# Kernel tuning notes

Measured on AMD Instinct MI355X. Metric: run time of the kernel, lower is better.

Reference implementation:

```python
import jax, jax.numpy as jnp
import numpy as np

N = 100_000  # nodes
E = 1_200_000  # edges (avg degree 12)
EPS = 1e-5


def setup_inputs() -> dict:
    key = jax.random.key(0)
    ks = jax.random.split(key, 12)

    def w(k, shape):
        fan_in = shape[0]
        return jax.random.normal(k, shape, dtype=jnp.float32) * (1.0 / np.sqrt(fan_in))

    return {
        "x": jax.random.normal(ks[0], (N, 4), dtype=jnp.float32),
        "edge_index": jax.random.randint(ks[1], (2, E), 0, N, dtype=jnp.int32),
        "W1": w(ks[2], (4, 16)), "b1": jnp.zeros(16, jnp.float32),
        "g1": jnp.ones(16, jnp.float32), "bt1": jnp.zeros(16, jnp.float32),
        "W2": w(ks[3], (16, 32)), "b2": jnp.zeros(32, jnp.float32),
        "g2": jnp.ones(32, jnp.float32), "bt2": jnp.zeros(32, jnp.float32),
        "W3": w(ks[4], (32, 64)), "b3": jnp.zeros(64, jnp.float32),
        "g3": jnp.ones(64, jnp.float32), "bt3": jnp.zeros(64, jnp.float32),
        "Wf1": w(ks[5], (64, 32)), "bf1": jnp.zeros(32, jnp.float32),
        "Wf2": w(ks[6], (32, 16)), "bf2": jnp.zeros(16, jnp.float32),
        "Wf3": w(ks[7], (16, 2)), "bf3": jnp.zeros(2, jnp.float32),
    }


def _gcn_conv(x, W, b, src, dst):
    """PyG GCNConv: self-loops + symmetric deg^-1/2 normalization + scatter-add."""
    n = x.shape[0]
    h = x @ W  # [N, out]
    loop = jnp.arange(n, dtype=src.dtype)
    s = jnp.concatenate([src, loop])  # [E+N]
    d = jnp.concatenate([dst, loop])
    deg = jax.ops.segment_sum(jnp.ones_like(d, dtype=h.dtype), d, num_segments=n)
    dinv = jnp.where(deg > 0, jax.lax.rsqrt(deg), 0.0)
    norm = dinv[s] * dinv[d]  # [E+N]
    out = jax.ops.segment_sum(h[s] * norm[:, None], d, num_segments=n)
    return out + b


def _bn(x, g, bt):
    # BatchNorm1d over node dim (batch statistics, training-mode semantics)
    m = jnp.mean(x, axis=0)
    v = jnp.var(x, axis=0)
    return (x - m) * jax.lax.rsqrt(v + EPS) * g + bt


def reference(x, edge_index, W1, b1, g1, bt1, W2, b2, g2, bt2, W3, b3, g3, bt3,
              Wf1, bf1, Wf2, bf2, Wf3, bf3):
    src, dst = edge_index[0], edge_index[1]
    h = jax.nn.elu(_bn(jax.nn.relu(_gcn_conv(x, W1, b1, src, dst)), g1, bt1))
    h = jax.nn.elu(_bn(jax.nn.relu(_gcn_conv(h, W2, b2, src, dst)), g2, bt2))
    h = jax.nn.elu(_bn(jax.nn.relu(_gcn_conv(h, W3, b3, src, dst)), g3, bt3))
    h = jax.nn.elu(h @ Wf1 + bf1)
    h = jax.nn.elu(h @ Wf2 + bf2)
    h = h @ Wf3 + bf3
    return jax.nn.log_softmax(h, axis=1)
```

## Files before the change

### kernel.cpp

```cpp
#include <hip/hip_runtime.h>
#include <hip/hip_fp16.h>
#include <math.h>

#define BN_EPS 1e-5f

union H8 {
  float4 f4;
  __half2 h2[4];
};


#define NHB 512

__global__ void hist_kernel(const int* __restrict__ dst, int* __restrict__ histpart, int e) {
  __shared__ int h[512];
  for (int i = threadIdx.x; i < 512; i += 256) h[i] = 0;
  __syncthreads();
  int stride = gridDim.x * 256;
  for (int i = blockIdx.x * 256 + threadIdx.x; i < e; i += stride)
    atomicAdd(&h[dst[i] >> 8], 1);
  __syncthreads();
  for (int i = threadIdx.x; i < 512; i += 256)
    histpart[blockIdx.x * 512 + i] = h[i];
}

__global__ void scan_buckets(const int* __restrict__ histpart,
                             int* __restrict__ boffset, int* __restrict__ bcursor,
                             int* __restrict__ row_start, int nbuck, int n, int e) {
  __shared__ int sc[512];
  int tid = threadIdx.x;
  int v = 0;
  for (int r = 0; r < NHB; r++) v += histpart[r * 512 + tid];
  sc[tid] = v;
  __syncthreads();
  for (int off = 1; off < 512; off <<= 1) {
    int add = (tid >= off) ? sc[tid - off] : 0;
    __syncthreads();
    sc[tid] += add;
    __syncthreads();
  }
  int excl = sc[tid] - v;
  if (tid <= nbuck) {
    int val = (tid < nbuck) ? excl : e;
    boffset[tid] = val;
    bcursor[tid] = val;
  }
  if (tid == 0) row_start[n] = e;
}

__global__ void partition_kernel(const int* __restrict__ src, const int* __restrict__ dst,
                                 int* __restrict__ bcursor, int* __restrict__ ebuf, int e) {
  __shared__ int h[512];
  __shared__ int base[512];
  const int BLK_E = 4096;
  int e0 = blockIdx.x * BLK_E;
  int e1 = min(e0 + BLK_E, e);
  for (int i = threadIdx.x; i < 512; i += 256) h[i] = 0;
  __syncthreads();
  for (int i = e0 + threadIdx.x; i < e1; i += 256)
    atomicAdd(&h[dst[i] >> 8], 1);
  __syncthreads();
  for (int i = threadIdx.x; i < 512; i += 256) {
    int c = h[i];
    base[i] = (c > 0) ? atomicAdd(&bcursor[i], c) : 0;
    h[i] = 0;
  }
  __syncthreads();
  for (int i = e0 + threadIdx.x; i < e1; i += 256) {
    int d = dst[i];
    int b = d >> 8;
    int r = atomicAdd(&h[b], 1);
    ebuf[base[b] + r] = (src[i] << 8) | (d & 255);
  }
}

__global__ void bucket_fill(const int* __restrict__ ebuf, const int* __restrict__ boffset,
                            int* __restrict__ row_start, float* __restrict__ dinv,
                            int* __restrict__ csr_src, int n) {
  __shared__ int lcnt[256];
  __shared__ int lpre[256];
  int bid = blockIdx.x;
  int nb0 = bid << 8;
  int tid = threadIdx.x;
  int e0 = boffset[bid], e1 = boffset[bid + 1];
  lcnt[tid] = 0;
  __syncthreads();
  for (int j = e0 + tid; j < e1; j += 256)
    atomicAdd(&lcnt[ebuf[j] & 255], 1);
  __syncthreads();
  int v = lcnt[tid];
  lpre[tid] = v;
  __syncthreads();
  for (int off = 1; off < 256; off <<= 1) {
    int add = (tid >= off) ? lpre[tid - off] : 0;
    __syncthreads();
    lpre[tid] += add;
    __syncthreads();
  }
  int excl = lpre[tid] - v;
  int node = nb0 + tid;
  if (node < n) {
    row_start[node] = e0 + excl;
    dinv[node] = rsqrtf((float)(v + 1));
  }
  __syncthreads();
  lpre[tid] = excl;
  __syncthreads();
  for (int j = e0 + tid; j < e1; j += 256) {
    int ed = ebuf[j];
    int p = atomicAdd(&lpre[ed & 255], 1);
    csr_src[e0 + p] = ed >> 8;
  }
}

template <int K, int C, bool BN>
__global__ __launch_bounds__(256) void mm_dinv_h(
    const float* __restrict__ X, const float* __restrict__ stats,
    const float* __restrict__ g, const float* __restrict__ bt,
    const float* __restrict__ W, const float* __restrict__ dinv,
    float4* __restrict__ hh, int n) {
  constexpr int GP8 = C / 8;
  __shared__ float w[K * C];
  __shared__ float bsc[K], bsh[K];
  for (int i = threadIdx.x; i < K * C; i += 256) w[i] = W[i];
  if (BN && threadIdx.x < K) {
    int c = threadIdx.x;
    float inv_n = 1.0f / (float)n;
    float m = stats[c] * inv_n;
    float var = fmaxf(stats[K + c] * inv_n - m * m, 0.f);
    float sc = rsqrtf(var + BN_EPS) * g[c];
    bsc[c] = sc;
    bsh[c] = bt[c] - m * sc;
  }
  __syncthreads();

  int idx = blockIdx.x * 256 + threadIdx.x;
  if (idx >= n * GP8) return;
  int nn = idx / GP8;
  int c8 = idx % GP8;

  float acc[8];
#pragma unroll
  for (int t = 0; t < 8; t++) acc[t] = 0.f;

  const float4* row4 = (const float4*)(X + (size_t)nn * K);
#pragma unroll
  for (int k4 = 0; k4 < K / 4; k4++) {
    float4 xv = row4[k4];
#pragma unroll
    for (int j = 0; j < 4; j++) {
      int k = k4 * 4 + j;
      float v = (j == 0) ? xv.x : (j == 1) ? xv.y : (j == 2) ? xv.z : xv.w;
      if (BN) {
        v = v * bsc[k] + bsh[k];
        v = v > 0.f ? v : (__expf(v) - 1.f);
      }
      int wb = k * C + c8 * 8;
#pragma unroll
      for (int t = 0; t < 8; t++) acc[t] += v * w[wb + t];
    }
  }
  float dn = dinv[nn];
  H8 o;
#pragma unroll
  for (int q = 0; q < 4; q++)
    o.h2[q] = __float22half2_rn(make_float2(acc[2 * q] * dn, acc[2 * q + 1] * dn));
  hh[idx] = o.f4;
}

template <int C, int LOGGP, bool OUTH>
__global__ __launch_bounds__(256) void gather_finalize_h(
    const float4* __restrict__ hh8, const int* __restrict__ row_start,
    const int* __restrict__ csr_src, const float* __restrict__ dinv,
    const float* __restrict__ bias, float4* __restrict__ act4,
    float* __restrict__ partials, int n) {
  constexpr int GP = C / 8;
  constexpr int GP4 = C / 4;
  constexpr int NPB = 256 / GP;
  int tid = threadIdx.x;
  int c8 = tid & (GP - 1);
  int local = tid >> LOGGP;
  int n0 = blockIdx.x * NPB + local;
  bool valid = (n0 < n);

  float vo[8];
#pragma unroll
  for (int t = 0; t < 8; t++) vo[t] = 0.f;

  if (valid) {
    float acc[8];
    {
      H8 u;
      u.f4 = hh8[n0 * GP + c8];
#pragma unroll
      for (int q = 0; q < 4; q++) {
        float2 f = __half22float2(u.h2[q]);
        acc[2 * q] = f.x;
        acc[2 * q + 1] = f.y;
      }
    }
    int s = row_start[n0], e0 = row_start[n0 + 1];
    int j = s;
    for (; j + 8 <= e0; j += 8) {
      H8 u[8];
#pragma unroll
      for (int m = 0; m < 8; m++) u[m].f4 = hh8[csr_src[j + m] * GP + c8];
#pragma unroll
      for (int m = 0; m < 8; m++)
#pragma unroll
        for (int q = 0; q < 4; q++) {
          float2 f = __half22float2(u[m].h2[q]);
          acc[2 * q] += f.x;
          acc[2 * q + 1] += f.y;
        }
    }
    for (; j + 4 <= e0; j += 4) {
      H8 u[4];
#pragma unroll
      for (int m = 0; m < 4; m++) u[m].f4 = hh8[csr_src[j + m] * GP + c8];
#pragma unroll
      for (int m = 0; m < 4; m++)
#pragma unroll
        for (int q = 0; q < 4; q++) {
          float2 f = __half22float2(u[m].h2[q]);
          acc[2 * q] += f.x;
          acc[2 * q + 1] += f.y;
        }
    }
    for (; j < e0; j++) {
      H8 u;
      u.f4 = hh8[csr_src[j] * GP + c8];
#pragma unroll
      for (int q = 0; q < 4; q++) {
        float2 f = __half22float2(u.h2[q]);
        acc[2 * q] += f.x;
        acc[2 * q + 1] += f.y;
      }
    }

    float dn = dinv[n0];
    const float4* bias4 = (const float4*)bias;
    float4 blo = bias4[c8 * 2], bhi = bias4[c8 * 2 + 1];
    vo[0] = fmaxf(dn * acc[0] + blo.x, 0.f);
    vo[1] = fmaxf(dn * acc[1] + blo.y, 0.f);
    vo[2] = fmaxf(dn * acc[2] + blo.z, 0.f);
    vo[3] = fmaxf(dn * acc[3] + blo.w, 0.f);
    vo[4] = fmaxf(dn * acc[4] + bhi.x, 0.f);
    vo[5] = fmaxf(dn * acc[5] + bhi.y, 0.f);
    vo[6] = fmaxf(dn * acc[6] + bhi.z, 0.f);
    vo[7] = fmaxf(dn * acc[7] + bhi.w, 0.f);
    if (OUTH) {
      H8 o;
#pragma unroll
      for (int q = 0; q < 4; q++)
        o.h2[q] = __float22half2_rn(make_float2(vo[2 * q], vo[2 * q + 1]));
      act4[(size_t)n0 * GP + c8] = o.f4;
    } else {
      act4[n0 * GP4 + c8 * 2] = make_float4(vo[0], vo[1], vo[2], vo[3]);
      act4[n0 * GP4 + c8 * 2 + 1] = make_float4(vo[4], vo[5], vo[6], vo[7]);
    }
  }

  __shared__ float redS[8 * 256];
  __shared__ float redQ[8 * 256];
#pragma unroll
  for (int t = 0; t < 8; t++) {
    redS[t * 256 + tid] = vo[t];
    redQ[t * 256 + tid] = vo[t] * vo[t];
  }
#pragma unroll
  for (int off = NPB / 2; off >= 1; off >>= 1) {
    __syncthreads();
    if (local < off) {
#pragma unroll
      for (int t = 0; t < 8; t++) {
        redS[t * 256 + tid] += redS[t * 256 + tid + off * GP];
        redQ[t * 256 + tid] += redQ[t * 256 + tid + off * GP];
      }
    }
  }
  __syncthreads();
  if (local == 0) {
#pragma unroll
    for (int t = 0; t < 8; t++) {
      partials[(size_t)blockIdx.x * 2 * C + c8 * 8 + t] = redS[t * 256 + tid];
      partials[(size_t)blockIdx.x * 2 * C + C + c8 * 8 + t] = redQ[t * 256 + tid];
    }
  }
}

template <int C2>
__global__ void reduce_partials(const float* __restrict__ partials,
                                float* __restrict__ stats, int rows) {
  int ch = blockIdx.x;
  float acc = 0.f;
  for (int r = threadIdx.x; r < rows; r += 256)
    acc += partials[(size_t)r * C2 + ch];
  __shared__ float red[256];
  red[threadIdx.x] = acc;
  __syncthreads();
#pragma unroll
  for (int off = 128; off >= 1; off >>= 1) {
    if (threadIdx.x < off) red[threadIdx.x] += red[threadIdx.x + off];
    __syncthreads();
  }
  if (threadIdx.x == 0) stats[ch] = red[0];
}


__global__ __launch_bounds__(256) void head_kernel(
    const float4* __restrict__ h16,
    const float* __restrict__ st3, const float* __restrict__ g3,
    const float* __restrict__ bt3,
    const float* __restrict__ Wf1, const float* __restrict__ bf1,
    const float* __restrict__ Wf2, const float* __restrict__ bf2,
    const float* __restrict__ Wf3, const float* __restrict__ bf3,
    float* __restrict__ out, int n) {
  __shared__ float w1[64 * 32], w2[32 * 16], w3[32];
  __shared__ float sb1[32], sb2[16], sb3[2];
  __shared__ float bsc[64], bsh[64];
  __shared__ float a1s[32][128];
  __shared__ float a2s[16][128];
  int tid = threadIdx.x;
  for (int i = tid; i < 64 * 32; i += 256) w1[i] = Wf1[i];
  for (int i = tid; i < 32 * 16; i += 256) w2[i] = Wf2[i];
  if (tid < 64) {
    float inv_n = 1.0f / (float)n;
    float m = st3[tid] * inv_n;
    float var = fmaxf(st3[64 + tid] * inv_n - m * m, 0.f);
    float sc = rsqrtf(var + BN_EPS) * g3[tid];
    bsc[tid] = sc;
    bsh[tid] = bt3[tid] - m * sc;
  }
  if (tid < 32) {
    w3[tid] = Wf3[tid];
    sb1[tid] = bf1[tid];
  }
  if (tid < 16) sb2[tid] = bf2[tid];
  if (tid < 2) sb3[tid] = bf3[tid];
  __syncthreads();

  int node = tid & 127;
  int half = tid >> 7;
  int n0 = blockIdx.x * 128 + node;
  bool valid = (n0 < n);

  float a1[16];
#pragma unroll
  for (int c = 0; c < 16; c++) a1[c] = sb1[half * 16 + c];
  if (valid) {
    const float4* hrow = h16 + (size_t)n0 * 8;
#pragma unroll
    for (int j = 0; j < 8; j++) {
      H8 u;
      u.f4 = hrow[j];
#pragma unroll
      for (int q = 0; q < 4; q++) {
        float2 f = __half22float2(u.h2[q]);
        int k0 = j * 8 + 2 * q, k1 = k0 + 1;
        float v0 = f.x * bsc[k0] + bsh[k0];
        v0 = v0 > 0.f ? v0 : (__expf(v0) - 1.f);
        float v1 = f.y * bsc[k1] + bsh[k1];
        v1 = v1 > 0.f ? v1 : (__expf(v1) - 1.f);
#pragma unroll
        for (int c = 0; c < 16; c++)
          a1[c] += v0 * w1[k0 * 32 + half * 16 + c] + v1 * w1[k1 * 32 + half * 16 + c];
      }
    }
  }
#pragma unroll
  for (int c = 0; c < 16; c++) {
    float v = a1[c];
    a1s[half * 16 + c][node] = v > 0.f ? v : (__expf(v) - 1.f);
  }
  __syncthreads();

  float a2[8];
#pragma unroll
  for (int c = 0; c < 8; c++) a2[c] = sb2[half * 8 + c];
#pragma unroll
  for (int k = 0; k < 32; k++) {
    float ak = a1s[k][node];
#pragma unroll
    for (int c = 0; c < 8; c++) a2[c] += ak * w2[k * 16 + half * 8 + c];
  }
#pragma unroll
  for (int c = 0; c < 8; c++) {
    float v = a2[c];
    a2s[half * 8 + c][node] = v > 0.f ? v : (__expf(v) - 1.f);
  }
  __syncthreads();

  if (half == 0 && valid) {
    float z0 = sb3[0], z1 = sb3[1];
#pragma unroll
    for (int k = 0; k < 16; k++) {
      float ak = a2s[k][node];
      z0 += ak * w3[k * 2 + 0];
      z1 += ak * w3[k * 2 + 1];
    }
    float mx = fmaxf(z0, z1);
    float lse = mx + __logf(__expf(z0 - mx) + __expf(z1 - mx));
    out[(size_t)n0 * 2 + 0] = z0 - lse;
    out[(size_t)n0 * 2 + 1] = z1 - lse;
  }
}


extern "C" void kernel_launch(void* const* d_in, const int* in_sizes, int n_in,
                              void* d_out, int out_size, void* d_ws, size_t ws_size,
                              hipStream_t stream) {
  const float* x = (const float*)d_in[0];
  const int* ei = (const int*)d_in[1];
  const float* W1 = (const float*)d_in[2];  const float* b1 = (const float*)d_in[3];
  const float* g1 = (const float*)d_in[4];  const float* bt1 = (const float*)d_in[5];
  const float* W2 = (const float*)d_in[6];  const float* b2 = (const float*)d_in[7];
  const float* g2 = (const float*)d_in[8];  const float* bt2 = (const float*)d_in[9];
  const float* W3 = (const float*)d_in[10]; const float* b3 = (const float*)d_in[11];
  const float* g3 = (const float*)d_in[12]; const float* bt3 = (const float*)d_in[13];
  const float* Wf1 = (const float*)d_in[14]; const float* bf1 = (const float*)d_in[15];
  const float* Wf2 = (const float*)d_in[16]; const float* bf2 = (const float*)d_in[17];
  const float* Wf3 = (const float*)d_in[18]; const float* bf3 = (const float*)d_in[19];
  float* out = (float*)d_out;

  const int N = in_sizes[0] / 4;
  const int E = in_sizes[1] / 2;
  const int* srcp = ei;
  const int* dstp = ei + E;
  const int NBUCK = (N + 255) >> 8;

  char* ws = (char*)d_ws;
  size_t off = 0;
  auto alloc = [&](size_t bytes) {
    off = (off + 255) & ~(size_t)255;
    size_t o = off;
    off += bytes;
    return o;
  };
  float* dinv      = (float*)(ws + alloc((size_t)N * 4));
  int*   row_start = (int*)  (ws + alloc((size_t)(N + 1) * 4));
  int*   histpart  = (int*)  (ws + alloc((size_t)NHB * 512 * 4));
  float* stats     = (float*)(ws + alloc((size_t)224 * 4));
  int*   boffset   = (int*)  (ws + alloc((size_t)513 * 4));
  int*   bcursor   = (int*)  (ws + alloc((size_t)513 * 4));
  int*   csr_src   = (int*)  (ws + alloc((size_t)E * 4));
  float* partials  = (float*)(ws + alloc((size_t)3200 * 128 * 4));
  float* bufH      = (float*)(ws + alloc((size_t)N * 64 * 2));
  float* bufAct    = (float*)(ws + alloc((size_t)N * 64 * 4));
  float* st1 = stats;
  float* st2 = stats + 32;
  float* st3 = stats + 96;
  int*   ebuf = (int*)bufH;

  hist_kernel<<<NHB, 256, 0, stream>>>(dstp, histpart, E);
  scan_buckets<<<1, 512, 0, stream>>>(histpart, boffset, bcursor, row_start, NBUCK, N, E);
  partition_kernel<<<(E + 4095) / 4096, 256, 0, stream>>>(srcp, dstp, bcursor, ebuf, E);
  bucket_fill<<<NBUCK, 256, 0, stream>>>(ebuf, boffset, row_start, dinv, csr_src, N);

  int g1n = (N + 127) / 128;
  mm_dinv_h<4, 16, false><<<(N * 2 + 255) / 256, 256, 0, stream>>>(
      x, nullptr, nullptr, nullptr, W1, dinv, (float4*)bufH, N);
  gather_finalize_h<16, 1, false><<<g1n, 256, 0, stream>>>(
      (const float4*)bufH, row_start, csr_src, dinv, b1, (float4*)bufAct, partials, N);
  reduce_partials<32><<<32, 256, 0, stream>>>(partials, st1, g1n);

  int g2n = (N + 63) / 64;
  mm_dinv_h<16, 32, true><<<(N * 4 + 255) / 256, 256, 0, stream>>>(
      bufAct, st1, g1, bt1, W2, dinv, (float4*)bufH, N);
  gather_finalize_h<32, 2, false><<<g2n, 256, 0, stream>>>(
      (const float4*)bufH, row_start, csr_src, dinv, b2, (float4*)bufAct, partials, N);
  reduce_partials<64><<<64, 256, 0, stream>>>(partials, st2, g2n);

  int g3n = (N + 31) / 32;
  mm_dinv_h<32, 64, true><<<(N * 8 + 255) / 256, 256, 0, stream>>>(
      bufAct, st2, g2, bt2, W3, dinv, (float4*)bufH, N);
  gather_finalize_h<64, 3, true><<<g3n, 256, 0, stream>>>(
      (const float4*)bufH, row_start, csr_src, dinv, b3, (float4*)bufAct, partials, N);
  reduce_partials<128><<<128, 256, 0, stream>>>(partials, st3, g3n);

  head_kernel<<<(N + 127) / 128, 256, 0, stream>>>(
      (const float4*)bufAct, st3, g3, bt3, Wf1, bf1, Wf2, bf2, Wf3, bf3, out, N);
}
```

Baseline: 198.4 us.

## Aggregate before matmul in GCN layers to gather narrower features

Uses linearity of the GCN aggregation to gather the input features (width K) before multiplying by W, rather than gathering the transformed features (width C). This halves the bytes moved per edge in each layer's gather. The layer-1 input scaling is folded into bucket_fill, and a separate prep_y kernel applies BN+ELU+dinv. BN statistics now come from a separate stats_h pass using atomics instead of per-block partials plus a reduce kernel. Activations are stored in fp16 throughout, which adds an extra read pass per layer for stats and prep.

```diff
diff --git a/kernel.cpp b/kernel.cpp
--- a/kernel.cpp
+++ b/kernel.cpp
@@ -8,6 +8,10 @@
   float4 f4;
   __half2 h2[4];
 };
+union H4 {
+  uint2 u2;
+  __half2 h2[2];
+};
 
 
 #define NHB 512
@@ -26,9 +30,11 @@
 
 __global__ void scan_buckets(const int* __restrict__ histpart,
                              int* __restrict__ boffset, int* __restrict__ bcursor,
-                             int* __restrict__ row_start, int nbuck, int n, int e) {
+                             int* __restrict__ row_start, float* __restrict__ stats,
+                             int nbuck, int n, int e) {
   __shared__ int sc[512];
   int tid = threadIdx.x;
+  if (tid < 224) stats[tid] = 0.f;
   int v = 0;
   for (int r = 0; r < NHB; r++) v += histpart[r * 512 + tid];
   sc[tid] = v;
@@ -75,8 +81,9 @@
 }
 
 __global__ void bucket_fill(const int* __restrict__ ebuf, const int* __restrict__ boffset,
+                            const float* __restrict__ x,
                             int* __restrict__ row_start, float* __restrict__ dinv,
-                            int* __restrict__ csr_src, int n) {
+                            int* __restrict__ csr_src, uint2* __restrict__ y1, int n) {
   __shared__ int lcnt[256];
   __shared__ int lpre[256];
   int bid = blockIdx.x;
@@ -101,7 +108,13 @@
   int node = nb0 + tid;
   if (node < n) {
     row_start[node] = e0 + excl;
-    dinv[node] = rsqrtf((float)(v + 1));
+    float dnv = rsqrtf((float)(v + 1));
+    dinv[node] = dnv;
+    float4 xr = ((const float4*)x)[node];
+    H4 o;
+    o.h2[0] = __float22half2_rn(make_float2(xr.x * dnv, xr.y * dnv));
+    o.h2[1] = __float22half2_rn(make_float2(xr.z * dnv, xr.w * dnv));
+    y1[node] = o.u2;
   }
   __syncthreads();
   lpre[tid] = excl;
@@ -113,198 +126,222 @@
   }
 }
 
-template <int K, int C, bool BN>
-__global__ __launch_bounds__(256) void mm_dinv_h(
-    const float* __restrict__ X, const float* __restrict__ stats,
-    const float* __restrict__ g, const float* __restrict__ bt,
-    const float* __restrict__ W, const float* __restrict__ dinv,
-    float4* __restrict__ hh, int n) {
-  constexpr int GP8 = C / 8;
-  __shared__ float w[K * C];
-  __shared__ float bsc[K], bsh[K];
-  for (int i = threadIdx.x; i < K * C; i += 256) w[i] = W[i];
-  if (BN && threadIdx.x < K) {
+template <int K, int C, int LOGG>
+__global__ __launch_bounds__(256) void gather_mm(
+    const void* __restrict__ yv, const int* __restrict__ row_start,
+    const int* __restrict__ csr_src, const float* __restrict__ dinv,
+    const float* __restrict__ Wg, const float* __restrict__ bias,
+    float4* __restrict__ act4, int n) {
+  constexpr int G = 1 << LOGG;
+  constexpr int NPB = 256 >> LOGG;
+  constexpr int KG = (K >= 8) ? K / 8 : 1;
+  __shared__ __align__(16) float w[K * C];
+  __shared__ float sb[C];
+  __shared__ float s_lds[K][NPB + 1];
+  int tid = threadIdx.x;
+  for (int i = tid; i < K * C; i += 256) w[i] = Wg[i];
+  if (tid < C) sb[tid] = bias[tid];
+  int g = tid & (G - 1);
+  int local = tid >> LOGG;
+  int n0 = blockIdx.x * NPB + local;
+  bool valid = (n0 < n);
+
+  if (K == 4) {
+    const uint2* y4 = (const uint2*)yv;
+    float s0 = 0.f, s1 = 0.f, s2 = 0.f, s3 = 0.f;
+    if (valid) {
+      H4 u;
+      u.u2 = y4[n0];
+      float2 a = __half22float2(u.h2[0]), b = __half22float2(u.h2[1]);
+      s0 = a.x; s1 = a.y; s2 = b.x; s3 = b.y;
+      int st = row_start[n0], e0 = row_start[n0 + 1];
+      int j = st;
+      for (; j + 8 <= e0; j += 8) {
+        H4 u8[8];
+#pragma unroll
+        for (int m = 0; m < 8; m++) u8[m].u2 = y4[csr_src[j + m]];
+#pragma unroll
+        for (int m = 0; m < 8; m++) {
+          float2 p = __half22float2(u8[m].h2[0]), q = __half22float2(u8[m].h2[1]);
+          s0 += p.x; s1 += p.y; s2 += q.x; s3 += q.y;
+        }
+      }
+      for (; j < e0; j++) {
+        H4 u1;
+        u1.u2 = y4[csr_src[j]];
+        float2 p = __half22float2(u1.h2[0]), q = __half22float2(u1.h2[1]);
+        s0 += p.x; s1 += p.y; s2 += q.x; s3 += q.y;
+      }
+    }
+    s_lds[0][local] = s0; s_lds[1][local] = s1;
+    s_lds[2][local] = s2; s_lds[3][local] = s3;
+  } else {
+    const float4* y8 = (const float4*)yv;
+    float s[8];
+#pragma unroll
+    for (int t = 0; t < 8; t++) s[t] = 0.f;
+    if (valid) {
+      H8 u;
+      u.f4 = y8[(size_t)n0 * KG + g];
+#pragma unroll
+      for (int q = 0; q < 4; q++) {
+        float2 f = __half22float2(u.h2[q]);
+        s[2 * q] = f.x; s[2 * q + 1] = f.y;
+      }
+      int st = row_start[n0], e0 = row_start[n0 + 1];
+      int j = st;
+      for (; j + 8 <= e0; j += 8) {
+        H8 u8[8];
+#pragma unroll
+        for (int m = 0; m < 8; m++) u8[m].f4 = y8[(size_t)csr_src[j + m] * KG + g];
+#pragma unroll
+        for (int m = 0; m < 8; m++)
+#pragma unroll
+          for (int q = 0; q < 4; q++) {
+            float2 f = __half22float2(u8[m].h2[q]);
+            s[2 * q] += f.x; s[2 * q + 1] += f.y;
+          }
+      }
+      for (; j + 4 <= e0; j += 4) {
+        H8 u4[4];
+#pragma unroll
+        for (int m = 0; m < 4; m++) u4[m].f4 = y8[(size_t)csr_src[j + m] * KG + g];
+#pragma unroll
+        for (int m = 0; m < 4; m++)
+#pragma unroll
+          for (int q = 0; q < 4; q++) {
+            float2 f = __half22float2(u4[m].h2[q]);
+            s[2 * q] += f.x; s[2 * q + 1] += f.y;
+          }
+      }
+      for (; j < e0; j++) {
+        H8 u1;
+        u1.f4 = y8[(size_t)csr_src[j] * KG + g];
+#pragma unroll
+        for (int q = 0; q < 4; q++) {
+          float2 f = __half22float2(u1.h2[q]);
+          s[2 * q] += f.x; s[2 * q + 1] += f.y;
+        }
+      }
+    }
+#pragma unroll
+    for (int t = 0; t < 8; t++) s_lds[g * 8 + t][local] = s[t];
+  }
+  __syncthreads();
+
+  if (!valid) return;
+  float dn = dinv[n0];
+  float acc[16];
+#pragma unroll
+  for (int c = 0; c < 16; c++) acc[c] = 0.f;
+#pragma unroll
+  for (int k = 0; k < K; k++) {
+    float ak = s_lds[k][local];
+    const float4* wr = (const float4*)&w[k * C + g * 16];
+    float4 w0 = wr[0], w1 = wr[1], w2 = wr[2], w3 = wr[3];
+    acc[0] += ak * w0.x;  acc[1] += ak * w0.y;  acc[2] += ak * w0.z;  acc[3] += ak * w0.w;
+    acc[4] += ak * w1.x;  acc[5] += ak * w1.y;  acc[6] += ak * w1.z;  acc[7] += ak * w1.w;
+    acc[8] += ak * w2.x;  acc[9] += ak * w2.y;  acc[10] += ak * w2.z; acc[11] += ak * w2.w;
+    acc[12] += ak * w3.x; acc[13] += ak * w3.y; acc[14] += ak * w3.z; acc[15] += ak * w3.w;
+  }
+  H8 o0, o1;
+#pragma unroll
+  for (int q = 0; q < 4; q++) {
+    float v0 = fmaxf(dn * acc[2 * q] + sb[g * 16 + 2 * q], 0.f);
+    float v1 = fmaxf(dn * acc[2 * q + 1] + sb[g * 16 + 2 * q + 1], 0.f);
+    o0.h2[q] = __float22half2_rn(make_float2(v0, v1));
+    float v2 = fmaxf(dn * acc[8 + 2 * q] + sb[g * 16 + 8 + 2 * q], 0.f);
+    float v3 = fmaxf(dn * acc[8 + 2 * q + 1] + sb[g * 16 + 8 + 2 * q + 1], 0.f);
+    o1.h2[q] = __float22half2_rn(make_float2(v2, v3));
+  }
+  act4[(size_t)n0 * (C / 8) + g * 2] = o0.f4;
+  act4[(size_t)n0 * (C / 8) + g * 2 + 1] = o1.f4;
+}
+
+template <int C>
+__global__ __launch_bounds__(256) void stats_h(const float4* __restrict__ act4,
+                                               float* __restrict__ stats, int n) {
+  constexpr int GP = C / 8;
+  constexpr int NPB = 256 / GP;
+  int tid = threadIdx.x;
+  int c8 = tid & (GP - 1);
+  int local = tid / GP;
+  float s[8], q[8];
+#pragma unroll
+  for (int t = 0; t < 8; t++) { s[t] = 0.f; q[t] = 0.f; }
+  for (int n0 = blockIdx.x * NPB + local; n0 < n; n0 += gridDim.x * NPB) {
+    H8 u;
+    u.f4 = act4[(size_t)n0 * GP + c8];
+#pragma unroll
+    for (int p = 0; p < 4; p++) {
+      float2 f = __half22float2(u.h2[p]);
+      s[2 * p] += f.x;      s[2 * p + 1] += f.y;
+      q[2 * p] += f.x * f.x; q[2 * p + 1] += f.y * f.y;
+    }
+  }
+  __shared__ float redS[8 * 256];
+  __shared__ float redQ[8 * 256];
+#pragma unroll
+  for (int t = 0; t < 8; t++) {
+    redS[t * 256 + tid] = s[t];
+    redQ[t * 256 + tid] = q[t];
+  }
+#pragma unroll
+  for (int off = NPB / 2; off >= 1; off >>= 1) {
+    __syncthreads();
+    if (local < off) {
+#pragma unroll
+      for (int t = 0; t < 8; t++) {
+        redS[t * 256 + tid] += redS[t * 256 + tid + off * GP];
+        redQ[t * 256 + tid] += redQ[t * 256 + tid + off * GP];
+      }
+    }
+  }
+  __syncthreads();
+  if (local == 0) {
+#pragma unroll
+    for (int t = 0; t < 8; t++) {
+      atomicAdd(&stats[c8 * 8 + t], redS[t * 256 + tid]);
+      atomicAdd(&stats[C + c8 * 8 + t], redQ[t * 256 + tid]);
+    }
+  }
+}
+
+template <int C>
+__global__ __launch_bounds__(256) void prep_y(
+    const float4* __restrict__ act4, const float* __restrict__ stats,
+    const float* __restrict__ gg, const float* __restrict__ bt,
+    const float* __restrict__ dinv, float4* __restrict__ y, int n) {
+  constexpr int GP = C / 8;
+  __shared__ float bsc[C], bsh[C];
+  if (threadIdx.x < C) {
     int c = threadIdx.x;
     float inv_n = 1.0f / (float)n;
     float m = stats[c] * inv_n;
-    float var = fmaxf(stats[K + c] * inv_n - m * m, 0.f);
-    float sc = rsqrtf(var + BN_EPS) * g[c];
+    float var = fmaxf(stats[C + c] * inv_n - m * m, 0.f);
+    float sc = rsqrtf(var + BN_EPS) * gg[c];
     bsc[c] = sc;
     bsh[c] = bt[c] - m * sc;
   }
   __syncthreads();
-
   int idx = blockIdx.x * 256 + threadIdx.x;
-  if (idx >= n * GP8) return;
-  int nn = idx / GP8;
-  int c8 = idx % GP8;
-
-  float acc[8];
-#pragma unroll
-  for (int t = 0; t < 8; t++) acc[t] = 0.f;
-
-  const float4* row4 = (const float4*)(X + (size_t)nn * K);
-#pragma unroll
-  for (int k4 = 0; k4 < K / 4; k4++) {
-    float4 xv = row4[k4];
-#pragma unroll
-    for (int j = 0; j < 4; j++) {
-      int k = k4 * 4 + j;
-      float v = (j == 0) ? xv.x : (j == 1) ? xv.y : (j == 2) ? xv.z : xv.w;
-      if (BN) {
-        v = v * bsc[k] + bsh[k];
-        v = v > 0.f ? v : (__expf(v) - 1.f);
-      }
-      int wb = k * C + c8 * 8;
-#pragma unroll
-      for (int t = 0; t < 8; t++) acc[t] += v * w[wb + t];
-    }
-  }
+  if (idx >= n * GP) return;
+  int nn = idx / GP;
+  int c8 = idx % GP;
   float dn = dinv[nn];
-  H8 o;
-#pragma unroll
-  for (int q = 0; q < 4; q++)
-    o.h2[q] = __float22half2_rn(make_float2(acc[2 * q] * dn, acc[2 * q + 1] * dn));
-  hh[idx] = o.f4;
-}
-
-template <int C, int LOGGP, bool OUTH>
-__global__ __launch_bounds__(256) void gather_finalize_h(
-    const float4* __restrict__ hh8, const int* __restrict__ row_start,
-    const int* __restrict__ csr_src, const float* __restrict__ dinv,
-    const float* __restrict__ bias, float4* __restrict__ act4,
-    float* __restrict__ partials, int n) {
-  constexpr int GP = C / 8;
-  constexpr int GP4 = C / 4;
-  constexpr int NPB = 256 / GP;
-  int tid = threadIdx.x;
-  int c8 = tid & (GP - 1);
-  int local = tid >> LOGGP;
-  int n0 = blockIdx.x * NPB + local;
-  bool valid = (n0 < n);
-
-  float vo[8];
-#pragma unroll
-  for (int t = 0; t < 8; t++) vo[t] = 0.f;
-
-  if (valid) {
-    float acc[8];
-    {
-      H8 u;
-      u.f4 = hh8[n0 * GP + c8];
-#pragma unroll
-      for (int q = 0; q < 4; q++) {
-        float2 f = __half22float2(u.h2[q]);
-        acc[2 * q] = f.x;
-        acc[2 * q + 1] = f.y;
-      }
-    }
-    int s = row_start[n0], e0 = row_start[n0 + 1];
-    int j = s;
-    for (; j + 8 <= e0; j += 8) {
-      H8 u[8];
-#pragma unroll
-      for (int m = 0; m < 8; m++) u[m].f4 = hh8[csr_src[j + m] * GP + c8];
-#pragma unroll
-      for (int m = 0; m < 8; m++)
-#pragma unroll
-        for (int q = 0; q < 4; q++) {
-          float2 f = __half22float2(u[m].h2[q]);
-          acc[2 * q] += f.x;
-          acc[2 * q + 1] += f.y;
-        }
-    }
-    for (; j + 4 <= e0; j += 4) {
-      H8 u[4];
-#pragma unroll
-      for (int m = 0; m < 4; m++) u[m].f4 = hh8[csr_src[j + m] * GP + c8];
-#pragma unroll
-      for (int m = 0; m < 4; m++)
-#pragma unroll
-        for (int q = 0; q < 4; q++) {
-          float2 f = __half22float2(u[m].h2[q]);
-          acc[2 * q] += f.x;
-          acc[2 * q + 1] += f.y;
-        }
-    }
-    for (; j < e0; j++) {
-      H8 u;
-      u.f4 = hh8[csr_src[j] * GP + c8];
-#pragma unroll
-      for (int q = 0; q < 4; q++) {
-        float2 f = __half22float2(u.h2[q]);
-        acc[2 * q] += f.x;
-        acc[2 * q + 1] += f.y;
-      }
-    }
-
-    float dn = dinv[n0];
-    const float4* bias4 = (const float4*)bias;
-    float4 blo = bias4[c8 * 2], bhi = bias4[c8 * 2 + 1];
-    vo[0] = fmaxf(dn * acc[0] + blo.x, 0.f);
-    vo[1] = fmaxf(dn * acc[1] + blo.y, 0.f);
-    vo[2] = fmaxf(dn * acc[2] + blo.z, 0.f);
-    vo[3] = fmaxf(dn * acc[3] + blo.w, 0.f);
-    vo[4] = fmaxf(dn * acc[4] + bhi.x, 0.f);
-    vo[5] = fmaxf(dn * acc[5] + bhi.y, 0.f);
-    vo[6] = fmaxf(dn * acc[6] + bhi.z, 0.f);
-    vo[7] = fmaxf(dn * acc[7] + bhi.w, 0.f);
-    if (OUTH) {
-      H8 o;
-#pragma unroll
-      for (int q = 0; q < 4; q++)
-        o.h2[q] = __float22half2_rn(make_float2(vo[2 * q], vo[2 * q + 1]));
-      act4[(size_t)n0 * GP + c8] = o.f4;
-    } else {
-      act4[n0 * GP4 + c8 * 2] = make_float4(vo[0], vo[1], vo[2], vo[3]);
-      act4[n0 * GP4 + c8 * 2 + 1] = make_float4(vo[4], vo[5], vo[6], vo[7]);
-    }
-  }
-
-  __shared__ float redS[8 * 256];
-  __shared__ float redQ[8 * 256];
-#pragma unroll
-  for (int t = 0; t < 8; t++) {
-    redS[t * 256 + tid] = vo[t];
-    redQ[t * 256 + tid] = vo[t] * vo[t];
-  }
-#pragma unroll
-  for (int off = NPB / 2; off >= 1; off >>= 1) {
-    __syncthreads();
-    if (local < off) {
-#pragma unroll
-      for (int t = 0; t < 8; t++) {
-        redS[t * 256 + tid] += redS[t * 256 + tid + off * GP];
-        redQ[t * 256 + tid] += redQ[t * 256 + tid + off * GP];
-      }
-    }
-  }
-  __syncthreads();
-  if (local == 0) {
-#pragma unroll
-    for (int t = 0; t < 8; t++) {
-      partials[(size_t)blockIdx.x * 2 * C + c8 * 8 + t] = redS[t * 256 + tid];
-      partials[(size_t)blockIdx.x * 2 * C + C + c8 * 8 + t] = redQ[t * 256 + tid];
-    }
-  }
-}
-
-template <int C2>
-__global__ void reduce_partials(const float* __restrict__ partials,
-                                float* __restrict__ stats, int rows) {
-  int ch = blockIdx.x;
-  float acc = 0.f;
-  for (int r = threadIdx.x; r < rows; r += 256)
-    acc += partials[(size_t)r * C2 + ch];
-  __shared__ float red[256];
-  red[threadIdx.x] = acc;
-  __syncthreads();
-#pragma unroll
-  for (int off = 128; off >= 1; off >>= 1) {
-    if (threadIdx.x < off) red[threadIdx.x] += red[threadIdx.x + off];
-    __syncthreads();
-  }
-  if (threadIdx.x == 0) stats[ch] = red[0];
+  H8 u, o;
+  u.f4 = act4[idx];
+#pragma unroll
+  for (int p = 0; p < 4; p++) {
+    float2 f = __half22float2(u.h2[p]);
+    int k0 = c8 * 8 + 2 * p, k1 = k0 + 1;
+    float v0 = f.x * bsc[k0] + bsh[k0];
+    v0 = v0 > 0.f ? v0 : (__expf(v0) - 1.f);
+    float v1 = f.y * bsc[k1] + bsh[k1];
+    v1 = v1 > 0.f ? v1 : (__expf(v1) - 1.f);
+    o.h2[p] = __float22half2_rn(make_float2(v0 * dn, v1 * dn));
+  }
+  y[idx] = o.f4;
 }
 
 
@@ -444,40 +481,36 @@
   int*   boffset   = (int*)  (ws + alloc((size_t)513 * 4));
   int*   bcursor   = (int*)  (ws + alloc((size_t)513 * 4));
   int*   csr_src   = (int*)  (ws + alloc((size_t)E * 4));
-  float* partials  = (float*)(ws + alloc((size_t)3200 * 128 * 4));
-  float* bufH      = (float*)(ws + alloc((size_t)N * 64 * 2));
-  float* bufAct    = (float*)(ws + alloc((size_t)N * 64 * 4));
+  uint2* y1        = (uint2*)(ws + alloc((size_t)N * 8));
+  float* ybuf      = (float*)(ws + alloc((size_t)N * 32 * 2));
+  float* act       = (float*)(ws + alloc((size_t)N * 64 * 2));
   float* st1 = stats;
   float* st2 = stats + 32;
   float* st3 = stats + 96;
-  int*   ebuf = (int*)bufH;
+  int*   ebuf = (int*)act;
 
   hist_kernel<<<NHB, 256, 0, stream>>>(dstp, histpart, E);
-  scan_buckets<<<1, 512, 0, stream>>>(histpart, boffset, bcursor, row_start, NBUCK, N, E);
+  scan_buckets<<<1, 512, 0, stream>>>(histpart, boffset, bcursor, row_start, stats,
+                                      NBUCK, N, E);
   partition_kernel<<<(E + 4095) / 4096, 256, 0, stream>>>(srcp, dstp, bcursor, ebuf, E);
-  bucket_fill<<<NBUCK, 256, 0, stream>>>(ebuf, boffset, row_start, dinv, csr_src, N);
-
-  int g1n = (N + 127) / 128;
-  mm_dinv_h<4, 16, false><<<(N * 2 + 255) / 256, 256, 0, stream>>>(
-      x, nullptr, nullptr, nullptr, W1, dinv, (float4*)bufH, N);
-  gather_finalize_h<16, 1, false><<<g1n, 256, 0, stream>>>(
-      (const float4*)bufH, row_start, csr_src, dinv, b1, (float4*)bufAct, partials, N);
-  reduce_partials<32><<<32, 256, 0, stream>>>(partials, st1, g1n);
-
-  int g2n = (N + 63) / 64;
-  mm_dinv_h<16, 32, true><<<(N * 4 + 255) / 256, 256, 0, stream>>>(
-      bufAct, st1, g1, bt1, W2, dinv, (float4*)bufH, N);
-  gather_finalize_h<32, 2, false><<<g2n, 256, 0, stream>>>(
-      (const float4*)bufH, row_start, csr_src, dinv, b2, (float4*)bufAct, partials, N);
-  reduce_partials<64><<<64, 256, 0, stream>>>(partials, st2, g2n);
-
-  int g3n = (N + 31) / 32;
-  mm_dinv_h<32, 64, true><<<(N * 8 + 255) / 256, 256, 0, stream>>>(
-      bufAct, st2, g2, bt2, W3, dinv, (float4*)bufH, N);
-  gather_finalize_h<64, 3, true><<<g3n, 256, 0, stream>>>(
-      (const float4*)bufH, row_start, csr_src, dinv, b3, (float4*)bufAct, partials, N);
-  reduce_partials<128><<<128, 256, 0, stream>>>(partials, st3, g3n);
+  bucket_fill<<<NBUCK, 256, 0, stream>>>(ebuf, boffset, x, row_start, dinv, csr_src, y1, N);
+
+  gather_mm<4, 16, 0><<<(N + 255) / 256, 256, 0, stream>>>(
+      y1, row_start, csr_src, dinv, W1, b1, (float4*)act, N);
+  stats_h<16><<<128, 256, 0, stream>>>((const float4*)act, st1, N);
+
+  prep_y<16><<<(N * 2 + 255) / 256, 256, 0, stream>>>(
+      (const float4*)act, st1, g1, bt1, dinv, (float4*)ybuf, N);
+  gather_mm<16, 32, 1><<<(N + 127) / 128, 256, 0, stream>>>(
+      ybuf, row_start, csr_src, dinv, W2, b2, (float4*)act, N);
+  stats_h<32><<<128, 256, 0, stream>>>((const float4*)act, st2, N);
+
+  prep_y<32><<<(N * 4 + 255) / 256, 256, 0, stream>>>(
+      (const float4*)act, st2, g2, bt2, dinv, (float4*)ybuf, N);
+  gather_mm<32, 64, 2><<<(N + 63) / 64, 256, 0, stream>>>(
+      ybuf, row_start, csr_src, dinv, W3, b3, (float4*)act, N);
+  stats_h<64><<<128, 256, 0, stream>>>((const float4*)act, st3, N);
 
   head_kernel<<<(N + 127) / 128, 256, 0, stream>>>(
-      (const float4*)bufAct, st3, g3, bt3, Wf1, bf1, Wf2, bf2, Wf3, bf3, out, N);
-}
+      (const float4*)act, st3, g3, bt3, Wf1, bf1, Wf2, bf2, Wf3, bf3, out, N);
+}
```

New measurement: 222.9 us. 12.4% more time.

## Fuse layer-1 matmul into bucket_fill and store all activations in fp16

Applied to the files above, without the earlier changes.

The first-layer x@W1 product, scaled by dinv, moves into bucket_fill, which computes dinv anyway, so the separate mm_dinv_h launch for layer 1 goes away. Layer-1 and layer-2 activations are now stored as fp16 instead of fp32, which halves the write and read traffic between the gather and matmul kernels. The edge buffer now aliases the activation buffer, because bufH is written inside bucket_fill. In exchange it adds fp16 rounding to the intermediate activations and extra register work in bucket_fill.

```diff
diff --git a/kernel.cpp b/kernel.cpp
--- a/kernel.cpp
+++ b/kernel.cpp
@@ -75,15 +75,18 @@
 }
 
 __global__ void bucket_fill(const int* __restrict__ ebuf, const int* __restrict__ boffset,
+                            const float* __restrict__ x, const float* __restrict__ W1,
                             int* __restrict__ row_start, float* __restrict__ dinv,
-                            int* __restrict__ csr_src, int n) {
+                            int* __restrict__ csr_src, float4* __restrict__ hh1, int n) {
   __shared__ int lcnt[256];
   __shared__ int lpre[256];
+  __shared__ float w1s[64];
   int bid = blockIdx.x;
   int nb0 = bid << 8;
   int tid = threadIdx.x;
   int e0 = boffset[bid], e1 = boffset[bid + 1];
   lcnt[tid] = 0;
+  if (tid < 64) w1s[tid] = W1[tid];
   __syncthreads();
   for (int j = e0 + tid; j < e1; j += 256)
     atomicAdd(&lcnt[ebuf[j] & 255], 1);
@@ -101,7 +104,21 @@
   int node = nb0 + tid;
   if (node < n) {
     row_start[node] = e0 + excl;
-    dinv[node] = rsqrtf((float)(v + 1));
+    float dnv = rsqrtf((float)(v + 1));
+    dinv[node] = dnv;
+    float4 xr = ((const float4*)x)[node];
+    float acc[16];
+#pragma unroll
+    for (int c = 0; c < 16; c++)
+      acc[c] = xr.x * w1s[c] + xr.y * w1s[16 + c] + xr.z * w1s[32 + c] + xr.w * w1s[48 + c];
+    H8 o0, o1;
+#pragma unroll
+    for (int q = 0; q < 4; q++) {
+      o0.h2[q] = __float22half2_rn(make_float2(acc[2 * q] * dnv, acc[2 * q + 1] * dnv));
+      o1.h2[q] = __float22half2_rn(make_float2(acc[8 + 2 * q] * dnv, acc[8 + 2 * q + 1] * dnv));
+    }
+    hh1[(size_t)node * 2] = o0.f4;
+    hh1[(size_t)node * 2 + 1] = o1.f4;
   }
   __syncthreads();
   lpre[tid] = excl;
@@ -113,17 +130,18 @@
   }
 }
 
-template <int K, int C, bool BN>
+template <int K, int C>
 __global__ __launch_bounds__(256) void mm_dinv_h(
-    const float* __restrict__ X, const float* __restrict__ stats,
+    const float4* __restrict__ Xh, const float* __restrict__ stats,
     const float* __restrict__ g, const float* __restrict__ bt,
     const float* __restrict__ W, const float* __restrict__ dinv,
     float4* __restrict__ hh, int n) {
   constexpr int GP8 = C / 8;
+  constexpr int KG8 = K / 8;
   __shared__ float w[K * C];
   __shared__ float bsc[K], bsh[K];
   for (int i = threadIdx.x; i < K * C; i += 256) w[i] = W[i];
-  if (BN && threadIdx.x < K) {
+  if (threadIdx.x < K) {
     int c = threadIdx.x;
     float inv_n = 1.0f / (float)n;
     float m = stats[c] * inv_n;
@@ -143,21 +161,22 @@
 #pragma unroll
   for (int t = 0; t < 8; t++) acc[t] = 0.f;
 
-  const float4* row4 = (const float4*)(X + (size_t)nn * K);
-#pragma unroll
-  for (int k4 = 0; k4 < K / 4; k4++) {
-    float4 xv = row4[k4];
-#pragma unroll
-    for (int j = 0; j < 4; j++) {
-      int k = k4 * 4 + j;
-      float v = (j == 0) ? xv.x : (j == 1) ? xv.y : (j == 2) ? xv.z : xv.w;
-      if (BN) {
-        v = v * bsc[k] + bsh[k];
-        v = v > 0.f ? v : (__expf(v) - 1.f);
-      }
-      int wb = k * C + c8 * 8;
-#pragma unroll
-      for (int t = 0; t < 8; t++) acc[t] += v * w[wb + t];
+  const float4* rowh = Xh + (size_t)nn * KG8;
+#pragma unroll
+  for (int j8 = 0; j8 < KG8; j8++) {
+    H8 u;
+    u.f4 = rowh[j8];
+#pragma unroll
+    for (int q = 0; q < 4; q++) {
+      float2 f = __half22float2(u.h2[q]);
+      int k0 = j8 * 8 + 2 * q, k1 = k0 + 1;
+      float v0 = f.x * bsc[k0] + bsh[k0];
+      v0 = v0 > 0.f ? v0 : (__expf(v0) - 1.f);
+      float v1 = f.y * bsc[k1] + bsh[k1];
+      v1 = v1 > 0.f ? v1 : (__expf(v1) - 1.f);
+      int wb0 = k0 * C + c8 * 8, wb1 = k1 * C + c8 * 8;
+#pragma unroll
+      for (int t = 0; t < 8; t++) acc[t] += v0 * w[wb0 + t] + v1 * w[wb1 + t];
     }
   }
   float dn = dinv[nn];
@@ -168,14 +187,13 @@
   hh[idx] = o.f4;
 }
 
-template <int C, int LOGGP, bool OUTH>
+template <int C, int LOGGP>
 __global__ __launch_bounds__(256) void gather_finalize_h(
     const float4* __restrict__ hh8, const int* __restrict__ row_start,
     const int* __restrict__ csr_src, const float* __restrict__ dinv,
     const float* __restrict__ bias, float4* __restrict__ act4,
     float* __restrict__ partials, int n) {
   constexpr int GP = C / 8;
-  constexpr int GP4 = C / 4;
   constexpr int NPB = 256 / GP;
   int tid = threadIdx.x;
   int c8 = tid & (GP - 1);
@@ -191,7 +209,7 @@
     float acc[8];
     {
       H8 u;
-      u.f4 = hh8[n0 * GP + c8];
+      u.f4 = hh8[(size_t)n0 * GP + c8];
 #pragma unroll
       for (int q = 0; q < 4; q++) {
         float2 f = __half22float2(u.h2[q]);
@@ -204,7 +222,7 @@
     for (; j + 8 <= e0; j += 8) {
       H8 u[8];
 #pragma unroll
-      for (int m = 0; m < 8; m++) u[m].f4 = hh8[csr_src[j + m] * GP + c8];
+      for (int m = 0; m < 8; m++) u[m].f4 = hh8[(size_t)csr_src[j + m] * GP + c8];
 #pragma unroll
       for (int m = 0; m < 8; m++)
 #pragma unroll
@@ -217,7 +235,7 @@
     for (; j + 4 <= e0; j += 4) {
       H8 u[4];
 #pragma unroll
-      for (int m = 0; m < 4; m++) u[m].f4 = hh8[csr_src[j + m] * GP + c8];
+      for (int m = 0; m < 4; m++) u[m].f4 = hh8[(size_t)csr_src[j + m] * GP + c8];
 #pragma unroll
       for (int m = 0; m < 4; m++)
 #pragma unroll
@@ -229,7 +247,7 @@
     }
     for (; j < e0; j++) {
       H8 u;
-      u.f4 = hh8[csr_src[j] * GP + c8];
+      u.f4 = hh8[(size_t)csr_src[j] * GP + c8];
 #pragma unroll
       for (int q = 0; q < 4; q++) {
         float2 f = __half22float2(u.h2[q]);
@@ -249,16 +267,11 @@
     vo[5] = fmaxf(dn * acc[5] + bhi.y, 0.f);
     vo[6] = fmaxf(dn * acc[6] + bhi.z, 0.f);
     vo[7] = fmaxf(dn * acc[7] + bhi.w, 0.f);
-    if (OUTH) {
-      H8 o;
-#pragma unroll
-      for (int q = 0; q < 4; q++)
-        o.h2[q] = __float22half2_rn(make_float2(vo[2 * q], vo[2 * q + 1]));
-      act4[(size_t)n0 * GP + c8] = o.f4;
-    } else {
-      act4[n0 * GP4 + c8 * 2] = make_float4(vo[0], vo[1], vo[2], vo[3]);
-      act4[n0 * GP4 + c8 * 2 + 1] = make_float4(vo[4], vo[5], vo[6], vo[7]);
-    }
+    H8 o;
+#pragma unroll
+    for (int q = 0; q < 4; q++)
+      o.h2[q] = __float22half2_rn(make_float2(vo[2 * q], vo[2 * q + 1]));
+    act4[(size_t)n0 * GP + c8] = o.f4;
   }
 
   __shared__ float redS[8 * 256];
@@ -446,35 +459,34 @@
   int*   csr_src   = (int*)  (ws + alloc((size_t)E * 4));
   float* partials  = (float*)(ws + alloc((size_t)3200 * 128 * 4));
   float* bufH      = (float*)(ws + alloc((size_t)N * 64 * 2));
-  float* bufAct    = (float*)(ws + alloc((size_t)N * 64 * 4));
+  float* bufAct    = (float*)(ws + alloc((size_t)N * 64 * 2));
   float* st1 = stats;
   float* st2 = stats + 32;
   float* st3 = stats + 96;
-  int*   ebuf = (int*)bufH;
+  int*   ebuf = (int*)bufAct;
 
   hist_kernel<<<NHB, 256, 0, stream>>>(dstp, histpart, E);
   scan_buckets<<<1, 512, 0, stream>>>(histpart, boffset, bcursor, row_start, NBUCK, N, E);
   partition_kernel<<<(E + 4095) / 4096, 256, 0, stream>>>(srcp, dstp, bcursor, ebuf, E);
-  bucket_fill<<<NBUCK, 256, 0, stream>>>(ebuf, boffset, row_start, dinv, csr_src, N);
+  bucket_fill<<<NBUCK, 256, 0, stream>>>(ebuf, boffset, x, W1, row_start, dinv, csr_src,
+                                         (float4*)bufH, N);
 
   int g1n = (N + 127) / 128;
-  mm_dinv_h<4, 16, false><<<(N * 2 + 255) / 256, 256, 0, stream>>>(
-      x, nullptr, nullptr, nullptr, W1, dinv, (float4*)bufH, N);
-  gather_finalize_h<16, 1, false><<<g1n, 256, 0, stream>>>(
+  gather_finalize_h<16, 1><<<g1n, 256, 0, stream>>>(
       (const float4*)bufH, row_start, csr_src, dinv, b1, (float4*)bufAct, partials, N);
   reduce_partials<32><<<32, 256, 0, stream>>>(partials, st1, g1n);
 
   int g2n = (N + 63) / 64;
-  mm_dinv_h<16, 32, true><<<(N * 4 + 255) / 256, 256, 0, stream>>>(
-      bufAct, st1, g1, bt1, W2, dinv, (float4*)bufH, N);
-  gather_finalize_h<32, 2, false><<<g2n, 256, 0, stream>>>(
+  mm_dinv_h<16, 32><<<(N * 4 + 255) / 256, 256, 0, stream>>>(
+      (const float4*)bufAct, st1, g1, bt1, W2, dinv, (float4*)bufH, N);
+  gather_finalize_h<32, 2><<<g2n, 256, 0, stream>>>(
       (const float4*)bufH, row_start, csr_src, dinv, b2, (float4*)bufAct, partials, N);
   reduce_partials<64><<<64, 256, 0, stream>>>(partials, st2, g2n);
 
   int g3n = (N + 31) / 32;
-  mm_dinv_h<32, 64, true><<<(N * 8 + 255) / 256, 256, 0, stream>>>(
-      bufAct, st2, g2, bt2, W3, dinv, (float4*)bufH, N);
-  gather_finalize_h<64, 3, true><<<g3n, 256, 0, stream>>>(
+  mm_dinv_h<32, 64><<<(N * 8 + 255) / 256, 256, 0, stream>>>(
+      (const float4*)bufAct, st2, g2, bt2, W3, dinv, (float4*)bufH, N);
+  gather_finalize_h<64, 3><<<g3n, 256, 0, stream>>>(
       (const float4*)bufH, row_start, csr_src, dinv, b3, (float4*)bufAct, partials, N);
   reduce_partials<128><<<128, 256, 0, stream>>>(partials, st3, g3n);
 
```

New measurement: 201.4 us, median of 3. About the same (+1.5%).
